# Optimization experiments

Hardware: AMD Instinct MI355X
Metric: run time of the kernel (lower is better)

Reference implementation:

```python
import jax, jax.numpy as jnp
import numpy as np

L = 28       # spectral bands
M = 256      # rows
N = 256      # cols (== patch_size, so phi crop is identity)
STRIDE = 2   # dispersion shift per band


def setup_inputs() -> dict:
    key = jax.random.key(0)
    kx, kp = jax.random.split(key)
    x = jax.random.normal(kx, (32, L, M, N), dtype=jnp.float32)
    # binary coded aperture: (1 + sign(randn)) / 2, repeated over bands
    phi2d = (1.0 + jnp.sign(jax.random.normal(kp, (M, N), dtype=jnp.float32))) / 2.0
    phi = jnp.broadcast_to(phi2d[None, :, :], (L, M, N)).astype(jnp.float32)
    return {"x": x, "phi": phi}


def reference(x, phi):
    """CASSI forward: A^T(A(x)) with coded-aperture mask phi.

    x:   [B, L, M, N] hyperspectral cube
    phi: [L, M, N]    coded aperture (binary mask)
    returns [B, L, M, N]
    """
    B = x.shape[0]
    n_out = N + STRIDE * (L - 1)  # dispersed measurement width (310)

    # --- get_measurement: mask then per-band shift-and-sum ---
    y1 = x * phi[None]  # einsum('blmn,lmn->blmn')
    # column index each (band l, col n) lands on after dispersion
    idx = (jnp.arange(N)[None, :] + STRIDE * jnp.arange(L)[:, None]).reshape(-1)  # [L*N]
    vals = jnp.transpose(y1, (0, 2, 1, 3)).reshape(B, M, L * N)  # [B, M, L*N]
    # fused shift-scatter-add instead of L pad+accumulate passes
    y2 = jnp.zeros((B, M, n_out), dtype=x.dtype).at[:, :, idx].add(vals)  # [B, M, 310]

    # --- get_transpose: gather shifted windows, re-mask ---
    xt = y2[:, :, idx].reshape(B, M, L, N)          # [B, M, L, N]
    xt = jnp.transpose(xt, (0, 2, 1, 3))            # [B, L, M, N]
    return xt * phi[None]
```

## Files before the change

kernel.cpp:

```cpp
#include <hip/hip_runtime.h>


constexpr int L_BANDS = 28;
constexpr int M_DIM   = 256;
constexpr int N_DIM   = 256;
constexpr int SHIFT   = 2;
constexpr int N_OUT   = N_DIM + SHIFT * (L_BANDS - 1);
constexpr int NPAIR   = N_OUT / 2;
constexpr int MN      = M_DIM * N_DIM;

typedef float v2f __attribute__((ext_vector_type(2)));

__global__ __launch_bounds__(320) void cassi_fwd_kernel(
    const float* __restrict__ x,
    const float* __restrict__ phi,
    float* __restrict__ out)
{
    const int t = threadIdx.x;
    const int r = (t >= 160) ? 1 : 0;
    const int p = t - 160 * r;
    if (p >= NPAIR) return;

    const int b  = blockIdx.x >> 7;
    const int m  = ((blockIdx.x & 127) << 1) + r;
    const int c0 = p << 1;

    const float* xb = x   + b * (L_BANDS * MN) + m * N_DIM;
    const float* pb = phi +                      m * N_DIM;
    float*       ob = out + b * (L_BANDS * MN) + m * N_DIM;

    v2f xr[L_BANDS];
    v2f pr[L_BANDS];

    #pragma unroll
    for (int l = 0; l < L_BANDS; ++l) {
        const int n0 = c0 - SHIFT * l;
        const bool v = (unsigned)n0 < (unsigned)(N_DIM - 1);
        if (v) {
            xr[l] = *(const v2f*)(xb + l * MN + n0);
            pr[l] = *(const v2f*)(pb + l * MN + n0);
        } else {
            xr[l] = (v2f)(0.0f);
            pr[l] = (v2f)(0.0f);
        }
    }

    v2f acc = (v2f)(0.0f);
    #pragma unroll
    for (int l = 0; l < L_BANDS; ++l) {
        acc += xr[l] * pr[l];
    }

    #pragma unroll
    for (int l = 0; l < L_BANDS; ++l) {
        const int n0 = c0 - SHIFT * l;
        if ((unsigned)n0 < (unsigned)(N_DIM - 1)) {
            v2f o = pr[l] * acc;
            __builtin_nontemporal_store(o, (v2f*)(ob + l * MN + n0));
        }
    }
}

extern "C" void kernel_launch(void* const* d_in, const int* in_sizes, int n_in,
                              void* d_out, int out_size, void* d_ws, size_t ws_size,
                              hipStream_t stream) {
    const float* x   = (const float*)d_in[0];
    const float* phi = (const float*)d_in[1];
    float*       out = (float*)d_out;

    const int B = in_sizes[0] / (L_BANDS * MN);

    dim3 grid(B * (M_DIM / 2));
    dim3 block(320);
    cassi_fwd_kernel<<<grid, block, 0, stream>>>(x, phi, out);
}
```

Measured before the change: 80.99 us.

## Stage dispersed measurement in shared memory and write output with 16-byte stores

Each block now writes its per-row dispersed sums into a swizzled shared-memory buffer, synchronizes, and then runs a second phase where threads emit the output with float4 stores and fresh float4 phi loads. Before, each thread wrote 8-byte nontemporal stores straight from registers. The goal is more fully coalesced, wider output writes and fewer live registers in the store phase. The cost is re-reading phi from global memory, a block barrier, and dropping the nontemporal store hint.

```diff
diff --git a/kernel.cpp b/kernel.cpp
--- a/kernel.cpp
+++ b/kernel.cpp
@@ -8,56 +8,74 @@
 constexpr int N_OUT   = N_DIM + SHIFT * (L_BANDS - 1);
 constexpr int NPAIR   = N_OUT / 2;
 constexpr int MN      = M_DIM * N_DIM;
+constexpr int Y2PAD   = 352;
+constexpr int P2UNITS = 2 * L_BANDS * (N_DIM / 4);
 
 typedef float v2f __attribute__((ext_vector_type(2)));
+typedef float v4f __attribute__((ext_vector_type(4)));
+
+__device__ __forceinline__ int swz(int w) { return w + (w >> 3); }
 
 __global__ __launch_bounds__(320) void cassi_fwd_kernel(
     const float* __restrict__ x,
     const float* __restrict__ phi,
     float* __restrict__ out)
 {
-    const int t = threadIdx.x;
-    const int r = (t >= 160) ? 1 : 0;
-    const int p = t - 160 * r;
-    if (p >= NPAIR) return;
+    __shared__ float y2s[2][Y2PAD];
 
+    const int t  = threadIdx.x;
+    const int r  = (t >= 160) ? 1 : 0;
+    const int p  = t - 160 * r;
     const int b  = blockIdx.x >> 7;
-    const int m  = ((blockIdx.x & 127) << 1) + r;
-    const int c0 = p << 1;
+    const int m0 = (blockIdx.x & 127) << 1;
 
-    const float* xb = x   + b * (L_BANDS * MN) + m * N_DIM;
-    const float* pb = phi +                      m * N_DIM;
-    float*       ob = out + b * (L_BANDS * MN) + m * N_DIM;
+    if (p < NPAIR) {
+        const int m  = m0 + r;
+        const int c0 = p << 1;
+        const float* xb = x   + b * (L_BANDS * MN) + m * N_DIM;
+        const float* pb = phi +                      m * N_DIM;
 
-    v2f xr[L_BANDS];
-    v2f pr[L_BANDS];
+        v2f xr[L_BANDS];
+        v2f pr[L_BANDS];
+        #pragma unroll
+        for (int l = 0; l < L_BANDS; ++l) {
+            const int n0 = c0 - SHIFT * l;
+            const bool v = (unsigned)n0 < (unsigned)(N_DIM - 1);
+            if (v) {
+                xr[l] = *(const v2f*)(xb + l * MN + n0);
+                pr[l] = *(const v2f*)(pb + l * MN + n0);
+            } else {
+                xr[l] = (v2f)(0.0f);
+                pr[l] = (v2f)(0.0f);
+            }
+        }
+        v2f acc = (v2f)(0.0f);
+        #pragma unroll
+        for (int l = 0; l < L_BANDS; ++l) {
+            acc += xr[l] * pr[l];
+        }
+        y2s[r][swz(c0)]     = acc.x;
+        y2s[r][swz(c0 + 1)] = acc.y;
+    }
+    __syncthreads();
 
-    #pragma unroll
-    for (int l = 0; l < L_BANDS; ++l) {
-        const int n0 = c0 - SHIFT * l;
-        const bool v = (unsigned)n0 < (unsigned)(N_DIM - 1);
-        if (v) {
-            xr[l] = *(const v2f*)(xb + l * MN + n0);
-            pr[l] = *(const v2f*)(pb + l * MN + n0);
-        } else {
-            xr[l] = (v2f)(0.0f);
-            pr[l] = (v2f)(0.0f);
-        }
-    }
+    float* ob = out + b * (L_BANDS * MN);
+    for (int u = t; u < P2UNITS; u += 320) {
+        const int rr = u / (L_BANDS * 64);
+        const int v  = u - rr * (L_BANDS * 64);
+        const int l  = v >> 6;
+        const int q  = v & 63;
+        const int n0 = q << 2;
+        const int m  = m0 + rr;
+        const int w  = n0 + SHIFT * l;
 
-    v2f acc = (v2f)(0.0f);
-    #pragma unroll
-    for (int l = 0; l < L_BANDS; ++l) {
-        acc += xr[l] * pr[l];
-    }
-
-    #pragma unroll
-    for (int l = 0; l < L_BANDS; ++l) {
-        const int n0 = c0 - SHIFT * l;
-        if ((unsigned)n0 < (unsigned)(N_DIM - 1)) {
-            v2f o = pr[l] * acc;
-            __builtin_nontemporal_store(o, (v2f*)(ob + l * MN + n0));
-        }
+        const v4f p4 = *(const v4f*)(phi + l * MN + m * N_DIM + n0);
+        v4f y4;
+        y4.x = y2s[rr][swz(w)];
+        y4.y = y2s[rr][swz(w + 1)];
+        y4.z = y2s[rr][swz(w + 2)];
+        y4.w = y2s[rr][swz(w + 3)];
+        *(v4f*)(ob + l * MN + m * N_DIM + n0) = p4 * y4;
     }
 }
 
```

Measured after the change: 121.4 us. 49.9% more time.
